# Performance work log

Hardware: AMD Instinct MI355X
Metric: run time of the kernel (lower is better)

## Reference

```python
import jax, jax.numpy as jnp
import numpy as np

B, S, T, C, H = 16, 64, 4096, 512, 8
D = C // H
NEG = jnp.float32(-1e30)


def setup_inputs() -> dict:
    key = jax.random.key(0)
    ks = jax.random.split(key, 12)
    x = jax.random.normal(ks[0], (1, C, 1), dtype=jnp.float32)
    eh = jax.random.normal(ks[1], (B, C, T), dtype=jnp.float32)
    # ragged shot boundaries -> fixed (B, S) start/end arrays, end > start
    bounds = jnp.sort(jax.random.randint(ks[2], (B, S + 1), 0, T), axis=-1)
    shot_starts = bounds[:, :-1].astype(jnp.int32)
    shot_ends = jnp.maximum(bounds[:, 1:], shot_starts + 1).astype(jnp.int32)
    sc = 1.0 / np.sqrt(C)
    Wq = jax.random.normal(ks[3], (C, C), dtype=jnp.float32) * sc
    bq = jnp.zeros((C,), dtype=jnp.float32)
    Wk = jax.random.normal(ks[4], (C, C), dtype=jnp.float32) * sc
    bk = jnp.zeros((C,), dtype=jnp.float32)
    Wv = jax.random.normal(ks[5], (C, C), dtype=jnp.float32) * sc
    bv = jnp.zeros((C,), dtype=jnp.float32)
    Wp = jax.random.normal(ks[6], (C, C), dtype=jnp.float32) * sc
    bp = jnp.zeros((C,), dtype=jnp.float32)
    return {"x": x, "encoder_hidden_states": eh, "shot_starts": shot_starts,
            "shot_ends": shot_ends, "Wq": Wq, "bq": bq, "Wk": Wk, "bk": bk,
            "Wv": Wv, "bv": bv, "Wp": Wp, "bp": bp}


def reference(x, encoder_hidden_states, shot_starts, shot_ends,
              Wq, bq, Wk, bk, Wv, bv, Wp, bp):
    scale = 1.0 / np.sqrt(D)
    # 1x1 conv == pointwise matmul over channels
    q = (Wq @ x[0] + bq[:, None])            # (C, 1)
    k = jnp.einsum('oc,bct->bot', Wk, encoder_hidden_states) + bk[None, :, None]
    v = jnp.einsum('oc,bct->bot', Wv, encoder_hidden_states) + bv[None, :, None]
    qh = q.reshape(H, D) * scale             # (H, D) single query per head
    kh = k.reshape(B, H, D, T)               # (B, H, D, T)
    vh = v.reshape(B, H, D, T).transpose(0, 1, 3, 2)  # (B, H, T, D)
    att = jnp.einsum('hd,bhdt->bht', qh, kh)          # (B, H, T)
    pos = jnp.arange(T)
    seg = (pos[None, None, :] >= shot_starts[:, :, None]) & \
          (pos[None, None, :] < shot_ends[:, :, None])  # (B, S, T)
    logits = jnp.where(seg[:, :, None, :], att[:, None, :, :], NEG)  # (B,S,H,T)
    p = jax.nn.softmax(logits, axis=-1)
    out = jnp.einsum('bsht,bhtd->bshd', p, vh)        # (B, S, H, D)
    out = out.reshape(B * S, C)
    out = out @ Wp.T + bp                              # proj (1x1 conv)
    return out[:, :, None]                             # (B*S, C, 1)
```

## Files before the change

kernel.cpp:

```cpp
#include <hip/hip_runtime.h>
#include <cstdint>
#include <cstddef>

#define B_ 16
#define S_ 64
#define T_ 4096
#define C_ 512
#define H_ 8

#define WS_QKT     0
#define WS_QB      4096
#define WS_QH      4104
#define WS_LG      4616
#define WS_CNT     12808
#define WS_CSEG    12824
#define WS_CIDX    14872
#define WS_CMUL    16920
#define WS_APART   18968
#define WS_WSUM    2116120
#define WS_ATTNOUT 6310424

__global__ void k_prep1(const float* __restrict__ x, const float* __restrict__ Wq,
                        const float* __restrict__ bq, float* __restrict__ qh_g) {
  __shared__ float xs[C_];
  __shared__ float red[256];
  int tid = threadIdx.x;
  xs[tid] = x[tid];
  xs[tid + 256] = x[tid + 256];
  __syncthreads();
  int r0 = blockIdx.x * 32;
  int rl = tid >> 3, sub = tid & 7;
  int r = r0 + rl;
  const float* wr = Wq + (size_t)r * C_ + sub * 64;
  const float* xp = xs + sub * 64;
  float s = 0.f;
#pragma unroll
  for (int i = 0; i < 64; i += 4) {
    float4 w = *(const float4*)(wr + i);
    s += w.x * xp[i] + w.y * xp[i + 1] + w.z * xp[i + 2] + w.w * xp[i + 3];
  }
  red[tid] = s;
  __syncthreads();
  if (sub == 0) {
    float tot = bq[r];
#pragma unroll
    for (int i = 0; i < 8; ++i) tot += red[rl * 8 + i];
    qh_g[r] = tot * 0.125f;
  }
}

__global__ void k_prep2(const float* __restrict__ qh_g,
                        const float* __restrict__ Wk,
                        const float* __restrict__ bk, float* __restrict__ qkT,
                        float* __restrict__ qb) {
  __shared__ float qhs[64];
  int tid = threadIdx.x;
  int h = blockIdx.x;
  if (tid < 64) qhs[tid] = qh_g[h * 64 + tid];
  __syncthreads();
  int c0 = tid, c1 = tid + 256;
  float s0 = 0.f, s1 = 0.f;
#pragma unroll 8
  for (int d = 0; d < 64; ++d) {
    const float* row = Wk + (size_t)(h * 64 + d) * C_;
    float q = qhs[d];
    s0 += q * row[c0];
    s1 += q * row[c1];
  }
  qkT[c0 * 8 + h] = s0;
  qkT[c1 * 8 + h] = s1;
  if (tid < 64) {
    float w = qhs[tid] * bk[h * 64 + tid];
#pragma unroll
    for (int off = 32; off > 0; off >>= 1) w += __shfl_down(w, off, 64);
    if (tid == 0) qb[h] = w;
  }
}

__global__ __launch_bounds__(256, 2) void k_att(
    const float* __restrict__ eh, const float* __restrict__ qkT,
    float* __restrict__ apart) {
  __shared__ float qks[C_ * 8];
  int tid = threadIdx.x;
  int tl = tid & 63, cg = tid >> 6;
  int b = blockIdx.y;
  int t0 = blockIdx.x * 128;
#pragma unroll
  for (int i = 0; i < 16; ++i) qks[tid + i * 256] = qkT[tid + i * 256];
  __syncthreads();
  const float* ehp = eh + ((size_t)b * C_ + (size_t)cg * 128) * T_ + t0 + tl;
  float acc0[8], acc1[8];
#pragma unroll
  for (int h = 0; h < 8; ++h) { acc0[h] = 0.f; acc1[h] = 0.f; }
#pragma unroll 4
  for (int j = 0; j < 128; ++j) {
    float e0 = ehp[(size_t)j * T_];
    float e1 = ehp[(size_t)j * T_ + 64];
    const float4 q0 = *(const float4*)&qks[(cg * 128 + j) * 8];
    const float4 q1 = *(const float4*)&qks[(cg * 128 + j) * 8 + 4];
    acc0[0] += q0.x * e0; acc0[1] += q0.y * e0; acc0[2] += q0.z * e0; acc0[3] += q0.w * e0;
    acc0[4] += q1.x * e0; acc0[5] += q1.y * e0; acc0[6] += q1.z * e0; acc0[7] += q1.w * e0;
    acc1[0] += q0.x * e1; acc1[1] += q0.y * e1; acc1[2] += q0.z * e1; acc1[3] += q0.w * e1;
    acc1[4] += q1.x * e1; acc1[5] += q1.y * e1; acc1[6] += q1.z * e1; acc1[7] += q1.w * e1;
  }
  float* ap = apart + (((size_t)cg * 16 + b) * 8) * T_ + t0 + tl;
#pragma unroll
  for (int h = 0; h < 8; ++h) {
    ap[(size_t)h * T_] = acc0[h];
    ap[(size_t)h * T_ + 64] = acc1[h];
  }
}

__global__ void k_map(const int* __restrict__ starts,
                      const int* __restrict__ ends, int* __restrict__ cnt,
                      int* __restrict__ cseg, int* __restrict__ cidx,
                      int* __restrict__ cmul) {
  int b = blockIdx.x;
  int s = threadIdx.x;
  int st = starts[b * 64 + s], en = ends[b * 64 + s];
  int cbase = st & ~31;
  int nch = (en - cbase + 127) >> 7;
  int x = nch;
#pragma unroll
  for (int off = 1; off < 64; off <<= 1) {
    int y = __shfl_up(x, off, 64);
    if (s >= off) x += y;
  }
  int pre = x - nch;
  for (int k = 0; k < nch; ++k) {
    cseg[b * 128 + pre + k] = s;
    cidx[b * 128 + pre + k] = k;
    cmul[b * 128 + pre + k] = (nch > 1) ? 1 : 0;
  }
  if (s == 63) cnt[b] = x;
}

__global__ __launch_bounds__(256, 2) void k_wsum(
    const float* __restrict__ eh, const float* __restrict__ apart,
    const float* __restrict__ qb, const int* __restrict__ starts,
    const int* __restrict__ ends, const int* __restrict__ cnt,
    const int* __restrict__ cseg, const int* __restrict__ cidx,
    const int* __restrict__ cmul, float* __restrict__ wsum,
    float* __restrict__ l_g) {
  __shared__ float pl[8 * 132];
  int b = blockIdx.y;
  int i = blockIdx.x;
  if (i >= cnt[b]) return;
  int tid = threadIdx.x;
  int s = cseg[b * 128 + i];
  int k = cidx[b * 128 + i];
  int mul = cmul[b * 128 + i];
  int n = b * 64 + s;
  int st = starts[n], en = ends[n];
  int cbase = st & ~31;
  int t_lo = cbase + k * 128;
  if (st > t_lo) t_lo = st;
  int t_hi = cbase + (k + 1) * 128;
  if (en < t_hi) t_hi = en;
  int base = t_lo & ~31;
  int span = t_hi - base;
  int jpad = (span + 31) & ~31;

#pragma unroll
  for (int r = 0; r < 4; ++r) {
    int idx = tid + r * 256;
    int h = idx >> 7, tt = idx & 127;
    int t = base + tt;
    float pv = 0.f;
    if (t >= t_lo && t < t_hi) {
      float a = qb[h];
      size_t o = ((size_t)b * 8 + h) * T_ + t;
      a += apart[o];
      a += apart[o + (size_t)128 * T_];
      a += apart[o + (size_t)256 * T_];
      a += apart[o + (size_t)384 * T_];
      pv = __expf(a);
    }
    pl[h * 132 + tt] = pv;
  }
  __syncthreads();

  if (tid < 64) {
    int h = tid >> 3, k8 = tid & 7;
    float ls = 0.f;
#pragma unroll
    for (int q = 0; q < 16; ++q) ls += pl[h * 132 + k8 * 16 + q];
    ls += __shfl_down(ls, 4, 8);
    ls += __shfl_down(ls, 2, 8);
    ls += __shfl_down(ls, 1, 8);
    if (k8 == 0) atomicAdd(&l_g[n * 8 + h], ls);
  }

  float acc0[8], acc1[8];
#pragma unroll
  for (int h = 0; h < 8; ++h) { acc0[h] = 0.f; acc1[h] = 0.f; }
  const float* e0p = eh + ((size_t)b * C_ + tid) * T_ + base;
  const float* e1p = e0p + (size_t)256 * T_;
  int nb = jpad >> 5;
  for (int jb = 0; jb < nb; ++jb) {
    int jo = jb * 32;
    float4 e0f[8], e1f[8];
#pragma unroll
    for (int q = 0; q < 8; ++q) e0f[q] = *(const float4*)(e0p + jo + q * 4);
#pragma unroll
    for (int q = 0; q < 8; ++q) e1f[q] = *(const float4*)(e1p + jo + q * 4);
#pragma unroll
    for (int t4 = 0; t4 < 8; ++t4) {
#pragma unroll
      for (int h = 0; h < 8; ++h) {
        const float4 p = *(const float4*)&pl[h * 132 + jo + t4 * 4];
        acc0[h] += p.x * e0f[t4].x + p.y * e0f[t4].y + p.z * e0f[t4].z +
                   p.w * e0f[t4].w;
        acc1[h] += p.x * e1f[t4].x + p.y * e1f[t4].y + p.z * e1f[t4].z +
                   p.w * e1f[t4].w;
      }
    }
  }
  float* wp = wsum + (size_t)n * (H_ * C_);
  if (!mul) {
#pragma unroll
    for (int h = 0; h < 8; ++h) {
      wp[h * C_ + tid] = acc0[h];
      wp[h * C_ + 256 + tid] = acc1[h];
    }
  } else {
#pragma unroll
    for (int h = 0; h < 8; ++h) {
      atomicAdd(&wp[h * C_ + tid], acc0[h]);
      atomicAdd(&wp[h * C_ + 256 + tid], acc1[h]);
    }
  }
}

__global__ __launch_bounds__(256, 4) void k_gemm(
    const float* __restrict__ A, long aRow, long aColPerY,
    const float* __restrict__ Bm, const float* __restrict__ bias,
    const float* __restrict__ l_g, float* __restrict__ Cc) {
  __shared__ float As[32 * 36];
  __shared__ float Bs[64 * 36];
  int tid = threadIdx.x;
  int n0 = blockIdx.x * 32;
  int y = blockIdx.y;
  const float* Abase = A + (size_t)n0 * aRow + (size_t)y * aColPerY;
  const float* Bbase = Bm + (size_t)(y * 64) * C_;
  int tx = tid & 15, ty = tid >> 4;
  float acc[2][4];
#pragma unroll
  for (int a = 0; a < 2; ++a)
#pragma unroll
    for (int bb = 0; bb < 4; ++bb) acc[a][bb] = 0.f;
  for (int k0 = 0; k0 < 512; k0 += 32) {
#pragma unroll
    for (int i = 0; i < 4; ++i) {
      int idx = tid + i * 256;
      int r = idx >> 5, cc = idx & 31;
      As[r * 36 + cc] = Abase[(size_t)r * aRow + k0 + cc];
    }
#pragma unroll
    for (int i = 0; i < 8; ++i) {
      int idx = tid + i * 256;
      int r = idx >> 5, cc = idx & 31;
      Bs[r * 36 + cc] = Bbase[(size_t)r * C_ + k0 + cc];
    }
    __syncthreads();
#pragma unroll
    for (int k = 0; k < 32; k += 4) {
      const float4 a0 = *(const float4*)&As[(ty * 2 + 0) * 36 + k];
      const float4 a1 = *(const float4*)&As[(ty * 2 + 1) * 36 + k];
#pragma unroll
      for (int bb = 0; bb < 4; ++bb) {
        const float4 bv = *(const float4*)&Bs[(tx * 4 + bb) * 36 + k];
        acc[0][bb] += a0.x * bv.x + a0.y * bv.y + a0.z * bv.z + a0.w * bv.w;
        acc[1][bb] += a1.x * bv.x + a1.y * bv.y + a1.z * bv.z + a1.w * bv.w;
      }
    }
    __syncthreads();
  }
#pragma unroll
  for (int a = 0; a < 2; ++a) {
    int nn = n0 + ty * 2 + a;
    float sc = l_g ? (1.0f / l_g[nn * 8 + y]) : 1.0f;
    float4 o;
    o.x = acc[a][0] * sc + bias[y * 64 + tx * 4 + 0];
    o.y = acc[a][1] * sc + bias[y * 64 + tx * 4 + 1];
    o.z = acc[a][2] * sc + bias[y * 64 + tx * 4 + 2];
    o.w = acc[a][3] * sc + bias[y * 64 + tx * 4 + 3];
    *(float4*)&Cc[(size_t)nn * C_ + y * 64 + tx * 4] = o;
  }
}

extern "C" void kernel_launch(void* const* d_in, const int* in_sizes, int n_in,
                              void* d_out, int out_size, void* d_ws,
                              size_t ws_size, hipStream_t stream) {
  const float* x = (const float*)d_in[0];
  const float* eh = (const float*)d_in[1];
  const int* shot_starts = (const int*)d_in[2];
  const int* shot_ends = (const int*)d_in[3];
  const float* Wq = (const float*)d_in[4];
  const float* bq = (const float*)d_in[5];
  const float* Wk = (const float*)d_in[6];
  const float* bk = (const float*)d_in[7];
  const float* Wv = (const float*)d_in[8];
  const float* bv = (const float*)d_in[9];
  const float* Wp = (const float*)d_in[10];
  const float* bp = (const float*)d_in[11];
  float* out = (float*)d_out;

  float* ws = (float*)d_ws;
  float* qkT = ws + WS_QKT;
  float* qb = ws + WS_QB;
  float* qh = ws + WS_QH;
  float* l_g = ws + WS_LG;
  int* cnt = (int*)(ws + WS_CNT);
  int* cseg = (int*)(ws + WS_CSEG);
  int* cidx = (int*)(ws + WS_CIDX);
  int* cmul = (int*)(ws + WS_CMUL);
  float* apart = ws + WS_APART;
  float* wsum = ws + WS_WSUM;
  float* attnout = ws + WS_ATTNOUT;

  hipMemsetAsync(wsum, 0, (size_t)1024 * H_ * C_ * sizeof(float), stream);
  hipMemsetAsync(l_g, 0, (size_t)1024 * H_ * sizeof(float), stream);
  k_prep1<<<16, 256, 0, stream>>>(x, Wq, bq, qh);
  k_prep2<<<8, 256, 0, stream>>>(qh, Wk, bk, qkT, qb);
  k_att<<<dim3(T_ / 128, B_), 256, 0, stream>>>(eh, qkT, apart);
  k_map<<<B_, 64, 0, stream>>>(shot_starts, shot_ends, cnt, cseg, cidx, cmul);
  k_wsum<<<dim3(128, B_), 256, 0, stream>>>(eh, apart, qb, shot_starts,
                                            shot_ends, cnt, cseg, cidx, cmul,
                                            wsum, l_g);
  k_gemm<<<dim3(32, 8), 256, 0, stream>>>(wsum, (long)(H_ * C_), (long)C_, Wv,
                                          bv, l_g, attnout);
  k_gemm<<<dim3(32, 8), 256, 0, stream>>>(attnout, (long)C_, 0L, Wp, bp,
                                          nullptr, out);
}
```

Baseline: 390.7 us.

## Fuse attention logits with transposed copy of encoder states for segment sums

The attention-logit kernel now reduces its channel partials in shared memory, adding the bias so it writes final logits. It also writes a transposed (T, C) copy of the encoder states. The weighted-sum kernel reads this transposed copy with contiguous rows per time step and uses 256-wide chunks aligned to each segment start instead of 32-aligned 128-wide ones. This is meant to remove the strided column loads and the four-way partial re-reads, at the cost of writing and re-reading an extra 128 MB buffer.

Result: slower. 404.7 us (+3.6%).

```diff
diff --git a/kernel.cpp b/kernel.cpp
--- a/kernel.cpp
+++ b/kernel.cpp
@@ -16,9 +16,10 @@
 #define WS_CSEG    12824
 #define WS_CIDX    14872
 #define WS_CMUL    16920
-#define WS_APART   18968
-#define WS_WSUM    2116120
-#define WS_ATTNOUT 6310424
+#define WS_ATT     18968
+#define WS_EHT     543256
+#define WS_WSUM    34097688
+#define WS_ATTNOUT 38291992
 
 __global__ void k_prep1(const float* __restrict__ x, const float* __restrict__ Wq,
                         const float* __restrict__ bq, float* __restrict__ qh_g) {
@@ -77,37 +78,55 @@
   }
 }
 
-__global__ __launch_bounds__(256, 2) void k_att(
+__global__ __launch_bounds__(256, 2) void k_atx(
     const float* __restrict__ eh, const float* __restrict__ qkT,
-    float* __restrict__ apart) {
+    const float* __restrict__ qb, float* __restrict__ att,
+    float* __restrict__ ehT) {
   __shared__ float qks[C_ * 8];
-  int tid = threadIdx.x;
-  int tl = tid & 63, cg = tid >> 6;
+  __shared__ float tile[64 * 130];
+  __shared__ float part[4 * 8 * 64];
+  int tid = threadIdx.x;
+  int tl = tid & 63, w = tid >> 6;
   int b = blockIdx.y;
-  int t0 = blockIdx.x * 128;
+  int t0 = blockIdx.x * 64;
 #pragma unroll
   for (int i = 0; i < 16; ++i) qks[tid + i * 256] = qkT[tid + i * 256];
   __syncthreads();
-  const float* ehp = eh + ((size_t)b * C_ + (size_t)cg * 128) * T_ + t0 + tl;
-  float acc0[8], acc1[8];
-#pragma unroll
-  for (int h = 0; h < 8; ++h) { acc0[h] = 0.f; acc1[h] = 0.f; }
-#pragma unroll 4
-  for (int j = 0; j < 128; ++j) {
-    float e0 = ehp[(size_t)j * T_];
-    float e1 = ehp[(size_t)j * T_ + 64];
-    const float4 q0 = *(const float4*)&qks[(cg * 128 + j) * 8];
-    const float4 q1 = *(const float4*)&qks[(cg * 128 + j) * 8 + 4];
-    acc0[0] += q0.x * e0; acc0[1] += q0.y * e0; acc0[2] += q0.z * e0; acc0[3] += q0.w * e0;
-    acc0[4] += q1.x * e0; acc0[5] += q1.y * e0; acc0[6] += q1.z * e0; acc0[7] += q1.w * e0;
-    acc1[0] += q0.x * e1; acc1[1] += q0.y * e1; acc1[2] += q0.z * e1; acc1[3] += q0.w * e1;
-    acc1[4] += q1.x * e1; acc1[5] += q1.y * e1; acc1[6] += q1.z * e1; acc1[7] += q1.w * e1;
-  }
-  float* ap = apart + (((size_t)cg * 16 + b) * 8) * T_ + t0 + tl;
-#pragma unroll
-  for (int h = 0; h < 8; ++h) {
-    ap[(size_t)h * T_] = acc0[h];
-    ap[(size_t)h * T_ + 64] = acc1[h];
+  float acc[8];
+#pragma unroll
+  for (int h = 0; h < 8; ++h) acc[h] = 0.f;
+  for (int g = 0; g < 4; ++g) {
+    const float* ehp = eh + ((size_t)b * C_ + g * 128 + w * 32) * T_ + t0 + tl;
+    const float* qp = qks + (g * 128 + w * 32) * 8;
+    float* tp = tile + tl * 130 + w * 32;
+#pragma unroll 8
+    for (int j = 0; j < 32; ++j) {
+      float e = ehp[(size_t)j * T_];
+      const float4 q0 = *(const float4*)&qp[j * 8];
+      const float4 q1 = *(const float4*)&qp[j * 8 + 4];
+      acc[0] += q0.x * e; acc[1] += q0.y * e; acc[2] += q0.z * e; acc[3] += q0.w * e;
+      acc[4] += q1.x * e; acc[5] += q1.y * e; acc[6] += q1.z * e; acc[7] += q1.w * e;
+      tp[j] = e;
+    }
+    __syncthreads();
+    float* eo = ehT + ((size_t)b * T_ + t0 + w * 16) * C_ + g * 128 + tl * 2;
+#pragma unroll
+    for (int r = 0; r < 16; ++r) {
+      float2 v = *(const float2*)&tile[(w * 16 + r) * 130 + tl * 2];
+      *(float2*)(eo + (size_t)r * C_) = v;
+    }
+    __syncthreads();
+  }
+#pragma unroll
+  for (int h = 0; h < 8; ++h) part[(w * 8 + h) * 64 + tl] = acc[h];
+  __syncthreads();
+#pragma unroll
+  for (int i = 0; i < 2; ++i) {
+    int idx = tid + i * 256;
+    int h = idx >> 6, tt = idx & 63;
+    float v = part[(0 * 8 + h) * 64 + tt] + part[(1 * 8 + h) * 64 + tt] +
+              part[(2 * 8 + h) * 64 + tt] + part[(3 * 8 + h) * 64 + tt] + qb[h];
+    att[((size_t)b * H_ + h) * T_ + t0 + tt] = v;
   }
 }
 
@@ -118,8 +137,7 @@
   int b = blockIdx.x;
   int s = threadIdx.x;
   int st = starts[b * 64 + s], en = ends[b * 64 + s];
-  int cbase = st & ~31;
-  int nch = (en - cbase + 127) >> 7;
+  int nch = (en - st + 255) >> 8;
   int x = nch;
 #pragma unroll
   for (int off = 1; off < 64; off <<= 1) {
@@ -135,14 +153,13 @@
   if (s == 63) cnt[b] = x;
 }
 
-__global__ __launch_bounds__(256, 2) void k_wsum(
-    const float* __restrict__ eh, const float* __restrict__ apart,
-    const float* __restrict__ qb, const int* __restrict__ starts,
-    const int* __restrict__ ends, const int* __restrict__ cnt,
-    const int* __restrict__ cseg, const int* __restrict__ cidx,
-    const int* __restrict__ cmul, float* __restrict__ wsum,
-    float* __restrict__ l_g) {
-  __shared__ float pl[8 * 132];
+__global__ __launch_bounds__(256, 4) void k_wsum(
+    const float* __restrict__ ehT, const float* __restrict__ att,
+    const int* __restrict__ starts, const int* __restrict__ ends,
+    const int* __restrict__ cnt, const int* __restrict__ cseg,
+    const int* __restrict__ cidx, const int* __restrict__ cmul,
+    float* __restrict__ wsum, float* __restrict__ l_g) {
+  __shared__ float pl[8 * 260];
   int b = blockIdx.y;
   int i = blockIdx.x;
   if (i >= cnt[b]) return;
@@ -152,31 +169,18 @@
   int mul = cmul[b * 128 + i];
   int n = b * 64 + s;
   int st = starts[n], en = ends[n];
-  int cbase = st & ~31;
-  int t_lo = cbase + k * 128;
-  if (st > t_lo) t_lo = st;
-  int t_hi = cbase + (k + 1) * 128;
-  if (en < t_hi) t_hi = en;
-  int base = t_lo & ~31;
-  int span = t_hi - base;
-  int jpad = (span + 31) & ~31;
-
-#pragma unroll
-  for (int r = 0; r < 4; ++r) {
+  int t_lo = st + k * 256;
+  int t_hi = t_lo + 256 < en ? t_lo + 256 : en;
+  int span = t_hi - t_lo;
+
+#pragma unroll
+  for (int r = 0; r < 8; ++r) {
     int idx = tid + r * 256;
-    int h = idx >> 7, tt = idx & 127;
-    int t = base + tt;
+    int h = idx >> 8, tt = idx & 255;
     float pv = 0.f;
-    if (t >= t_lo && t < t_hi) {
-      float a = qb[h];
-      size_t o = ((size_t)b * 8 + h) * T_ + t;
-      a += apart[o];
-      a += apart[o + (size_t)128 * T_];
-      a += apart[o + (size_t)256 * T_];
-      a += apart[o + (size_t)384 * T_];
-      pv = __expf(a);
-    }
-    pl[h * 132 + tt] = pv;
+    if (tt < span)
+      pv = __expf(att[((size_t)b * H_ + h) * T_ + t_lo + tt]);
+    pl[h * 260 + tt] = pv;
   }
   __syncthreads();
 
@@ -184,50 +188,48 @@
     int h = tid >> 3, k8 = tid & 7;
     float ls = 0.f;
 #pragma unroll
-    for (int q = 0; q < 16; ++q) ls += pl[h * 132 + k8 * 16 + q];
+    for (int q = 0; q < 32; ++q) ls += pl[h * 260 + k8 * 32 + q];
     ls += __shfl_down(ls, 4, 8);
     ls += __shfl_down(ls, 2, 8);
     ls += __shfl_down(ls, 1, 8);
     if (k8 == 0) atomicAdd(&l_g[n * 8 + h], ls);
   }
 
-  float acc0[8], acc1[8];
-#pragma unroll
-  for (int h = 0; h < 8; ++h) { acc0[h] = 0.f; acc1[h] = 0.f; }
-  const float* e0p = eh + ((size_t)b * C_ + tid) * T_ + base;
-  const float* e1p = e0p + (size_t)256 * T_;
-  int nb = jpad >> 5;
-  for (int jb = 0; jb < nb; ++jb) {
-    int jo = jb * 32;
-    float4 e0f[8], e1f[8];
-#pragma unroll
-    for (int q = 0; q < 8; ++q) e0f[q] = *(const float4*)(e0p + jo + q * 4);
-#pragma unroll
-    for (int q = 0; q < 8; ++q) e1f[q] = *(const float4*)(e1p + jo + q * 4);
-#pragma unroll
-    for (int t4 = 0; t4 < 8; ++t4) {
-#pragma unroll
-      for (int h = 0; h < 8; ++h) {
-        const float4 p = *(const float4*)&pl[h * 132 + jo + t4 * 4];
-        acc0[h] += p.x * e0f[t4].x + p.y * e0f[t4].y + p.z * e0f[t4].z +
-                   p.w * e0f[t4].w;
-        acc1[h] += p.x * e1f[t4].x + p.y * e1f[t4].y + p.z * e1f[t4].z +
-                   p.w * e1f[t4].w;
-      }
-    }
-  }
-  float* wp = wsum + (size_t)n * (H_ * C_);
+  float2 acc[8];
+#pragma unroll
+  for (int h = 0; h < 8; ++h) { acc[h].x = 0.f; acc[h].y = 0.f; }
+  const float* ep = ehT + ((size_t)b * T_ + t_lo) * C_ + tid * 2;
+  int j = 0;
+  for (; j + 4 <= span; j += 4) {
+    float2 e0 = *(const float2*)(ep + (size_t)(j + 0) * C_);
+    float2 e1 = *(const float2*)(ep + (size_t)(j + 1) * C_);
+    float2 e2 = *(const float2*)(ep + (size_t)(j + 2) * C_);
+    float2 e3 = *(const float2*)(ep + (size_t)(j + 3) * C_);
+#pragma unroll
+    for (int h = 0; h < 8; ++h) {
+      const float4 p = *(const float4*)&pl[h * 260 + j];
+      acc[h].x += p.x * e0.x + p.y * e1.x + p.z * e2.x + p.w * e3.x;
+      acc[h].y += p.x * e0.y + p.y * e1.y + p.z * e2.y + p.w * e3.y;
+    }
+  }
+  for (; j < span; ++j) {
+    float2 e = *(const float2*)(ep + (size_t)j * C_);
+#pragma unroll
+    for (int h = 0; h < 8; ++h) {
+      float p = pl[h * 260 + j];
+      acc[h].x += p * e.x;
+      acc[h].y += p * e.y;
+    }
+  }
+  float* wp = wsum + (size_t)n * (H_ * C_) + tid * 2;
   if (!mul) {
 #pragma unroll
+    for (int h = 0; h < 8; ++h) *(float2*)&wp[h * C_] = acc[h];
+  } else {
+#pragma unroll
     for (int h = 0; h < 8; ++h) {
-      wp[h * C_ + tid] = acc0[h];
-      wp[h * C_ + 256 + tid] = acc1[h];
-    }
-  } else {
-#pragma unroll
-    for (int h = 0; h < 8; ++h) {
-      atomicAdd(&wp[h * C_ + tid], acc0[h]);
-      atomicAdd(&wp[h * C_ + 256 + tid], acc1[h]);
+      atomicAdd(&wp[h * C_], acc[h].x);
+      atomicAdd(&wp[h * C_ + 1], acc[h].y);
     }
   }
 }
@@ -315,7 +317,8 @@
   int* cseg = (int*)(ws + WS_CSEG);
   int* cidx = (int*)(ws + WS_CIDX);
   int* cmul = (int*)(ws + WS_CMUL);
-  float* apart = ws + WS_APART;
+  float* att = ws + WS_ATT;
+  float* ehT = ws + WS_EHT;
   float* wsum = ws + WS_WSUM;
   float* attnout = ws + WS_ATTNOUT;
 
@@ -323,11 +326,10 @@
   hipMemsetAsync(l_g, 0, (size_t)1024 * H_ * sizeof(float), stream);
   k_prep1<<<16, 256, 0, stream>>>(x, Wq, bq, qh);
   k_prep2<<<8, 256, 0, stream>>>(qh, Wk, bk, qkT, qb);
-  k_att<<<dim3(T_ / 128, B_), 256, 0, stream>>>(eh, qkT, apart);
+  k_atx<<<dim3(T_ / 64, B_), 256, 0, stream>>>(eh, qkT, qb, att, ehT);
   k_map<<<B_, 64, 0, stream>>>(shot_starts, shot_ends, cnt, cseg, cidx, cmul);
-  k_wsum<<<dim3(128, B_), 256, 0, stream>>>(eh, apart, qb, shot_starts,
-                                            shot_ends, cnt, cseg, cidx, cmul,
-                                            wsum, l_g);
+  k_wsum<<<dim3(128, B_), 256, 0, stream>>>(ehT, att, shot_starts, shot_ends,
+                                            cnt, cseg, cidx, cmul, wsum, l_g);
   k_gemm<<<dim3(32, 8), 256, 0, stream>>>(wsum, (long)(H_ * C_), (long)C_, Wv,
                                           bv, l_g, attnout);
   k_gemm<<<dim3(32, 8), 256, 0, stream>>>(attnout, (long)C_, 0L, Wp, bp,
```
